# Kernel tuning notes

Measured on AMD Instinct MI355X. Metric: run time of the kernel, lower is better.

## Reference

```python
import jax, jax.numpy as jnp
import numpy as np

D = 512        # input_dim
C = 100        # n_classes
T = 15         # n_trees
DEPTH = 4      # tree_depth
H = 5          # n_heads
ENC = 64       # encoder_dim
GEN = 128      # generator hidden
N_INT = 2 ** DEPTH - 1   # 15 internal nodes
N_LEAF = 2 ** DEPTH      # 16 leaves
TOTAL = T * N_INT * (D + 1) + T * N_LEAF * C + T  # 139440
N_SUP, N_QRY = 4096, 32768


def setup_inputs() -> dict:
    key = jax.random.key(0)
    ks = jax.random.split(key, 8)
    s = lambda k, shp, sc: jax.random.normal(k, shp, jnp.float32) * sc
    return {
        "X_support": s(ks[0], (N_SUP, D), 1.0),
        "X_query": s(ks[1], (N_QRY, D), 1.0),
        # encoder per head: Linear(D,ENC) -> LayerNorm -> GELU -> Linear(ENC,ENC)
        "enc_w1": s(ks[2], (H, D, ENC), 0.5 / np.sqrt(D)),
        "enc_b1": jnp.zeros((H, ENC), jnp.float32),
        "ln_g": jnp.ones((H, ENC), jnp.float32),
        "ln_b": jnp.zeros((H, ENC), jnp.float32),
        "enc_w2": s(ks[3], (H, ENC, ENC), 0.5 / np.sqrt(ENC)),
        "enc_b2": jnp.zeros((H, ENC), jnp.float32),
        # generator per head: Linear(ENC,GEN) -> GELU -> Linear(GEN,TOTAL)
        "gen_w1": s(ks[4], (H, ENC, GEN), 0.5 / np.sqrt(ENC)),
        "gen_b1": jnp.zeros((H, GEN), jnp.float32),
        "gen_w2": s(ks[5], (H, GEN, TOTAL), 0.5 / np.sqrt(GEN)),
        "gen_b2": jnp.zeros((H, TOTAL), jnp.float32),
        "head_weights": jnp.ones((H,), jnp.float32) / H,
        "temperature": jnp.float32(1.0),
    }


def reference(X_support, X_query, enc_w1, enc_b1, ln_g, ln_b, enc_w2, enc_b2,
              gen_w1, gen_b1, gen_w2, gen_b2, head_weights, temperature):
    gelu = lambda x: jax.nn.gelu(x, approximate=False)  # torch nn.GELU default (erf)

    # ---- per-head encoder on support set: [H, S, ENC]
    h1 = jnp.einsum('sd,hde->hse', X_support, enc_w1) + enc_b1[:, None]
    mu = h1.mean(-1, keepdims=True)
    var = h1.var(-1, keepdims=True)  # biased, matches torch LayerNorm
    h1 = (h1 - mu) / jnp.sqrt(var + 1e-5) * ln_g[:, None] + ln_b[:, None]
    enc = jnp.einsum('hse,hef->hsf', gelu(h1), enc_w2) + enc_b2[:, None]
    ctx = enc.mean(axis=1)  # [H, ENC]  (mean over support dim, keepdim squeezed)

    # ---- per-head generator -> tree parameters
    g = gelu(jnp.einsum('he,heg->hg', ctx, gen_w1) + gen_b1)
    params = jnp.tanh(jnp.einsum('hg,hgp->hp', g, gen_w2) + gen_b2) * 2.0  # [H, TOTAL]

    i0 = T * N_INT * D
    i1 = i0 + T * N_INT
    i2 = i1 + T * N_LEAF * C
    split_w = params[:, :i0].reshape(H, T, N_INT, D)
    split_b = params[:, i0:i1].reshape(H, T, N_INT)
    leaf_logits = params[:, i1:i2].reshape(H, T, N_LEAF, C)
    tree_w = jax.nn.softmax(params[:, i2:i2 + T], axis=-1)  # [H, T]

    temp = jnp.clip(temperature, 0.1, 2.0)

    # ---- all node decisions in one pass: [H, Q, T, N_INT]
    dec = jax.nn.sigmoid(
        (jnp.einsum('qd,htnd->hqtn', X_query, split_w) + split_b[:, None]) / temp)

    # ---- bitwise reach propagation level by level (fixed DEPTH=4 loop)
    Q = X_query.shape[0]
    reach = jnp.ones((H, Q, T, 1), X_query.dtype)
    for d in range(DEPTH):
        n = 2 ** d
        start = n - 1
        dlev = dec[..., start:start + n]  # [H,Q,T,n]
        # interleave (left, right) per parent, matching torch new_reach ordering
        reach = jnp.stack([reach * (1.0 - dlev), reach * dlev], axis=-1)
        reach = reach.reshape(H, Q, T, 2 * n)
    # reach: [H, Q, T, N_LEAF]

    leaf_probs = jax.nn.softmax(leaf_logits / temp, axis=-1)  # [H,T,L,C]
    hw = jax.nn.softmax(head_weights)
    # fuse tree mixing and head mixing into one contraction -> [Q, C]
    return jnp.einsum('hqtl,htlc,ht,h->qc', reach, leaf_probs, tree_w, hw)
```

## Files before the change

kernel.cpp:

```cpp
#include <hip/hip_runtime.h>


#define TOTAL 139440
#define I0 115200
#define I1 115425
#define I2 139425
#define NPAIR 38

typedef _Float16 f16;
typedef _Float16 f16x8 __attribute__((ext_vector_type(8)));
typedef _Float16 f16x4 __attribute__((ext_vector_type(4)));
typedef float f32x16 __attribute__((ext_vector_type(16)));

__global__ __launch_bounds__(256) void k1_encode(
    const float* __restrict__ Xs, const float* __restrict__ w1,
    const float* __restrict__ b1, const float* __restrict__ lng,
    const float* __restrict__ lnb, const float* __restrict__ w2,
    float* __restrict__ ctx_sum)
{
  const int h = blockIdx.y;
  const int tid = threadIdx.x;
  const int lane = tid & 63;
  const int wave = tid >> 6;
  const int s0 = blockIdx.x * 64 + wave * 16;
  __shared__ float lsg[4][64];

  float w2r[64];
  #pragma unroll
  for (int e = 0; e < 64; ++e) w2r[e] = w2[(h * 64 + e) * 64 + lane];

  float acc[16];
  #pragma unroll
  for (int r = 0; r < 16; ++r) acc[r] = 0.f;

  const float* wp = w1 + h * 512 * 64;
  for (int d4 = 0; d4 < 128; ++d4) {
    const int d = d4 * 4;
    const float wa = wp[(d + 0) * 64 + lane];
    const float wb = wp[(d + 1) * 64 + lane];
    const float wc = wp[(d + 2) * 64 + lane];
    const float wd = wp[(d + 3) * 64 + lane];
    #pragma unroll
    for (int r = 0; r < 16; ++r) {
      const float4 x4 = *(const float4*)(Xs + (s0 + r) * 512 + d);
      acc[r] = fmaf(x4.x, wa, acc[r]);
      acc[r] = fmaf(x4.y, wb, acc[r]);
      acc[r] = fmaf(x4.z, wc, acc[r]);
      acc[r] = fmaf(x4.w, wd, acc[r]);
    }
  }

  const float bb = b1[h * 64 + lane];
  const float ge = lng[h * 64 + lane];
  const float be = lnb[h * 64 + lane];
  float ctxacc = 0.f;

  for (int r = 0; r < 16; ++r) {
    const float v = acc[r] + bb;
    float s = v, s2 = v * v;
    #pragma unroll
    for (int m = 1; m < 64; m <<= 1) {
      s  += __shfl_xor(s, m, 64);
      s2 += __shfl_xor(s2, m, 64);
    }
    const float mu = s * (1.f / 64.f);
    const float var = fmaxf(s2 * (1.f / 64.f) - mu * mu, 0.f);
    const float y = (v - mu) * rsqrtf(var + 1e-5f) * ge + be;
    const float gl = 0.5f * y * (1.f + erff(y * 0.70710678118654752f));
    lsg[wave][lane] = gl;
    float sm = 0.f;
    #pragma unroll
    for (int e4 = 0; e4 < 16; ++e4) {
      const float4 g4 = *(const float4*)(&lsg[wave][e4 * 4]);
      sm = fmaf(g4.x, w2r[e4 * 4 + 0], sm);
      sm = fmaf(g4.y, w2r[e4 * 4 + 1], sm);
      sm = fmaf(g4.z, w2r[e4 * 4 + 2], sm);
      sm = fmaf(g4.w, w2r[e4 * 4 + 3], sm);
    }
    ctxacc += sm;
  }
  atomicAdd(&ctx_sum[h * 64 + lane], ctxacc);
}

__global__ __launch_bounds__(256) void k2_ctx(
    const float* __restrict__ eb2, const float* __restrict__ gw1,
    const float* __restrict__ gb1, const float* __restrict__ hwin,
    const float* __restrict__ tempin, const float* __restrict__ ctx_sum,
    float* __restrict__ g_out, float* __restrict__ hwit)
{
  __shared__ float ctx[320];
  const int tid = threadIdx.x;
  for (int i = tid; i < 320; i += 256)
    ctx[i] = ctx_sum[i] * (1.f / 4096.f) + eb2[i];
  __syncthreads();
  for (int i = tid; i < 640; i += 256) {
    const int h = i >> 7, j = i & 127;
    float a = gb1[i];
    for (int e = 0; e < 64; ++e)
      a = fmaf(ctx[h * 64 + e], gw1[(h * 64 + e) * 128 + j], a);
    g_out[i] = 0.5f * a * (1.f + erff(a * 0.70710678118654752f));
  }
  if (tid == 0) {
    float m = hwin[0];
    for (int i = 1; i < 5; ++i) m = fmaxf(m, hwin[i]);
    float ex[5]; float se = 0.f;
    for (int i = 0; i < 5; ++i) { ex[i] = __expf(hwin[i] - m); se += ex[i]; }
    for (int i = 0; i < 5; ++i) hwit[i] = ex[i] / se;
    float tp = tempin[0];
    tp = fminf(fmaxf(tp, 0.1f), 2.0f);
    hwit[5] = 1.0f / tp;
  }
}

__global__ __launch_bounds__(256) void k3_params(
    const float* __restrict__ gv, const float* __restrict__ gw2,
    const float* __restrict__ gb2, float* __restrict__ params)
{
  const int h = blockIdx.y;
  __shared__ float gl[128];
  const int tid = threadIdx.x;
  if (tid < 128) gl[tid] = gv[h * 128 + tid];
  __syncthreads();
  const long i4 = (long)blockIdx.x * 256 + tid;
  if (i4 >= TOTAL / 4) return;
  const long i = i4 * 4;
  const float* wp = gw2 + (long)h * 128 * TOTAL + i;
  float4 a = *(const float4*)(gb2 + (long)h * TOTAL + i);
  #pragma unroll 4
  for (int k = 0; k < 128; ++k) {
    const float4 w4 = *(const float4*)(wp + (long)k * TOTAL);
    const float gk = gl[k];
    a.x = fmaf(gk, w4.x, a.x);
    a.y = fmaf(gk, w4.y, a.y);
    a.z = fmaf(gk, w4.z, a.z);
    a.w = fmaf(gk, w4.w, a.w);
  }
  float4 o;
  o.x = 2.f * tanhf(a.x);
  o.y = 2.f * tanhf(a.y);
  o.z = 2.f * tanhf(a.z);
  o.w = 2.f * tanhf(a.w);
  *(float4*)(params + (long)h * TOTAL + i) = o;
}

__global__ __launch_bounds__(256) void k4a_packw(
    const float* __restrict__ params, f16* __restrict__ wpk)
{
  const int t0 = blockIdx.x * 256 + threadIdx.x;
  const int lane = t0 & 63;
  const int kk = (t0 >> 6) & 31;
  const int pair = t0 >> 11;
  const int cl = lane & 31;
  const int tree = pair * 2 + (cl >> 4);
  const int n = cl & 15;
  f16x8 v;
  if (tree < 75 && n < 15) {
    const int h = tree / 15;
    const int t = tree - h * 15;
    const int dbase = kk * 16 + (lane >> 5) * 8;
    const float* src = params + (long)h * TOTAL + ((t * 15 + n) * 512 + dbase);
    const float4 x0 = *(const float4*)(src);
    const float4 x1 = *(const float4*)(src + 4);
    v[0] = (f16)x0.x; v[1] = (f16)x0.y; v[2] = (f16)x0.z; v[3] = (f16)x0.w;
    v[4] = (f16)x1.x; v[5] = (f16)x1.y; v[6] = (f16)x1.z; v[7] = (f16)x1.w;
  } else {
    #pragma unroll
    for (int j = 0; j < 8; ++j) v[j] = (f16)0.f;
  }
  *(f16x8*)(wpk + (long)t0 * 8) = v;
}

__global__ __launch_bounds__(128) void k4b_w2(
    const float* __restrict__ params, const float* __restrict__ hwit,
    f16* __restrict__ w2pk)
{
  const int g = blockIdx.x >> 4;
  const int leaf = blockIdx.x & 15;
  const int h = g / 15, t = g - h * 15;
  const float it = hwit[5];
  float m = -1e30f;
  float tl[15];
  #pragma unroll
  for (int i = 0; i < 15; ++i) {
    tl[i] = params[(long)h * TOTAL + I2 + i];
    m = fmaxf(m, tl[i]);
  }
  float se = 0.f;
  #pragma unroll
  for (int i = 0; i < 15; ++i) se += __expf(tl[i] - m);
  const float tw = __expf(tl[t] - m) / se;
  const float scale = tw * hwit[h];

  const int c = threadIdx.x;
  __shared__ float red[128];
  float lg = -1e30f;
  if (c < 100) lg = params[(long)h * TOTAL + I1 + ((t * 16 + leaf) * 100 + c)] * it;
  red[c] = lg;
  __syncthreads();
  for (int s = 64; s > 0; s >>= 1) {
    if (c < s) red[c] = fmaxf(red[c], red[c + s]);
    __syncthreads();
  }
  const float mx = red[0];
  __syncthreads();
  const float exv = (c < 100) ? __expf(lg - mx) : 0.f;
  red[c] = exv;
  __syncthreads();
  for (int s = 64; s > 0; s >>= 1) {
    if (c < s) red[c] += red[c + s];
    __syncthreads();
  }
  const float inv = 1.f / red[0];
  if (c < 100) {
    const float val = exv * inv * scale;
    const int ln = ((leaf >> 3) << 5) | (c & 31);
    const int j = leaf & 7;
    const int ct = c >> 5;
    w2pk[(((long)g * 4 + ct) * 64 + ln) * 8 + j] = (f16)val;
  }
}

__global__ __launch_bounds__(256, 2) void k5_query(
    const float* __restrict__ Xq, const float* __restrict__ params,
    const f16* __restrict__ wpk, const f16* __restrict__ w2pk,
    const float* __restrict__ hwit, float* __restrict__ out)
{
  __shared__ __align__(16) f16 xf[32 * 64 * 8];
  __shared__ float decs[4][32][34];
  __shared__ float ored[4][1024];

  const int tid = threadIdx.x;
  const int lane = tid & 63;
  const int wave = tid >> 6;
  const int qbase = blockIdx.x * 32;
  const float it = hwit[5];
  const int col = lane & 31;
  const int khalf = lane >> 5;

  {
    const int q = tid >> 3;
    const int db = (tid & 7) * 4;
    const float* xr = Xq + (long)(qbase + q) * 512;
    #pragma unroll
    for (int i = 0; i < 16; ++i) {
      const int d = db + i * 32;
      const float4 x4 = *(const float4*)(xr + d);
      const int kk = d >> 4;
      const int ln = q + 32 * ((d & 15) >> 3);
      const int j0 = d & 7;
      f16x4 v;
      v[0] = (f16)x4.x; v[1] = (f16)x4.y; v[2] = (f16)x4.z; v[3] = (f16)x4.w;
      *(f16x4*)(&xf[(kk * 64 + ln) * 8 + j0]) = v;
    }
  }
  __syncthreads();

  f32x16 oacc[4];
  #pragma unroll
  for (int ct = 0; ct < 4; ++ct)
    #pragma unroll
    for (int r = 0; r < 16; ++r) oacc[ct][r] = 0.f;

  auto process = [&](const f32x16& S0, const f32x16& S1, int pp) {
    const int tree = pp * 2 + (col >> 4);
    const int treec = (tree < 75) ? tree : 74;
    const int hh2 = treec / 15;
    const int tt2 = treec - hh2 * 15;
    const float bn = params[(long)hh2 * TOTAL + I0 + tt2 * 15 + (col & 15)];
    #pragma unroll
    for (int r = 0; r < 16; ++r) {
      const float z = (S0[r] + S1[r] + bn) * it;
      const float dv = 1.f / (1.f + __expf(-z));
      const int row = (r & 3) + 8 * (r >> 2) + 4 * khalf;
      decs[wave][row][col] = dv;
    }
    #pragma unroll
    for (int tf = 0; tf < 2; ++tf) {
      const int g = pp * 2 + tf;
      if (g < 75) {
        const int cb = tf * 16;
        const float* dsr = &decs[wave][col][cb];
        const float d0v = dsr[0];
        const float f0 = khalf ? d0v : 1.f - d0v;
        const float d1v = dsr[1 + khalf];
        const float p10 = f0 * (1.f - d1v);
        const float p11 = f0 * d1v;
        const float d2a = dsr[3 + 2 * khalf];
        const float d2b = dsr[4 + 2 * khalf];
        float p2[4];
        p2[0] = p10 * (1.f - d2a);
        p2[1] = p10 * d2a;
        p2[2] = p11 * (1.f - d2b);
        p2[3] = p11 * d2b;
        float d3[4];
        #pragma unroll
        for (int u = 0; u < 4; ++u) d3[u] = dsr[7 + 4 * khalf + u];
        f16x8 rf;
        #pragma unroll
        for (int mm = 0; mm < 8; ++mm) {
          const float rv = p2[mm >> 1] * ((mm & 1) ? d3[mm >> 1] : (1.f - d3[mm >> 1]));
          rf[mm] = (f16)rv;
        }
        const f16x8* w2p = (const f16x8*)w2pk + ((long)g * 4) * 64 + lane;
        oacc[0] = __builtin_amdgcn_mfma_f32_32x32x16_f16(rf, w2p[0],   oacc[0], 0, 0, 0);
        oacc[1] = __builtin_amdgcn_mfma_f32_32x32x16_f16(rf, w2p[64],  oacc[1], 0, 0, 0);
        oacc[2] = __builtin_amdgcn_mfma_f32_32x32x16_f16(rf, w2p[128], oacc[2], 0, 0, 0);
        oacc[3] = __builtin_amdgcn_mfma_f32_32x32x16_f16(rf, w2p[192], oacc[3], 0, 0, 0);
      }
    }
  };

  for (int p = wave; p < NPAIR; p += 8) {
    const bool has2 = (p + 4 < NPAIR);
    const f16x8* wha = (const f16x8*)wpk + (long)p * 32 * 64 + lane;
    const f16x8* whb = has2 ? ((const f16x8*)wpk + (long)(p + 4) * 32 * 64 + lane) : wha;
    f32x16 Sa0, Sa1, Sb0, Sb1;
    #pragma unroll
    for (int r = 0; r < 16; ++r) { Sa0[r] = 0.f; Sa1[r] = 0.f; Sb0[r] = 0.f; Sb1[r] = 0.f; }
    #pragma unroll
    for (int kk = 0; kk < 32; kk += 2) {
      const f16x8 af0 = *(const f16x8*)(&xf[(kk * 64 + lane) * 8]);
      const f16x8 af1 = *(const f16x8*)(&xf[((kk + 1) * 64 + lane) * 8]);
      const f16x8 wa0 = wha[(long)kk * 64];
      const f16x8 wa1 = wha[(long)(kk + 1) * 64];
      const f16x8 wb0 = whb[(long)kk * 64];
      const f16x8 wb1 = whb[(long)(kk + 1) * 64];
      Sa0 = __builtin_amdgcn_mfma_f32_32x32x16_f16(af0, wa0, Sa0, 0, 0, 0);
      Sb0 = __builtin_amdgcn_mfma_f32_32x32x16_f16(af0, wb0, Sb0, 0, 0, 0);
      Sa1 = __builtin_amdgcn_mfma_f32_32x32x16_f16(af1, wa1, Sa1, 0, 0, 0);
      Sb1 = __builtin_amdgcn_mfma_f32_32x32x16_f16(af1, wb1, Sb1, 0, 0, 0);
    }
    process(Sa0, Sa1, p);
    if (has2) process(Sb0, Sb1, p + 4);
  }

  __syncthreads();
  #pragma unroll
  for (int ct = 0; ct < 4; ++ct) {
    #pragma unroll
    for (int r = 0; r < 16; ++r) {
      const int row = (r & 3) + 8 * (r >> 2) + 4 * khalf;
      ored[wave][row * 32 + col] = oacc[ct][r];
    }
    __syncthreads();
    for (int e = tid; e < 1024; e += 256) {
      const float sm = ored[0][e] + ored[1][e] + ored[2][e] + ored[3][e];
      const int q = e >> 5;
      const int c = ct * 32 + (e & 31);
      if (c < 100) out[(long)(qbase + q) * 100 + c] = sm;
    }
    __syncthreads();
  }
}

extern "C" void kernel_launch(void* const* d_in, const int* in_sizes, int n_in,
                              void* d_out, int out_size, void* d_ws, size_t ws_size,
                              hipStream_t stream) {
  (void)in_sizes; (void)n_in; (void)out_size; (void)ws_size;
  const float* Xs  = (const float*)d_in[0];
  const float* Xq  = (const float*)d_in[1];
  const float* ew1 = (const float*)d_in[2];
  const float* eb1 = (const float*)d_in[3];
  const float* lng = (const float*)d_in[4];
  const float* lnb = (const float*)d_in[5];
  const float* ew2 = (const float*)d_in[6];
  const float* eb2 = (const float*)d_in[7];
  const float* gw1 = (const float*)d_in[8];
  const float* gb1 = (const float*)d_in[9];
  const float* gw2 = (const float*)d_in[10];
  const float* gb2 = (const float*)d_in[11];
  const float* hwi = (const float*)d_in[12];
  const float* tmp = (const float*)d_in[13];
  float* out = (float*)d_out;

  char* ws = (char*)d_ws;
  float* params = (float*)(ws);
  f16*   wpk    = (f16*)(ws + 2788800);
  f16*   w2pk   = (f16*)(ws + 2788800 + 1245184);
  float* ctxs   = (float*)(ws + 4341184);
  float* gbuf   = (float*)(ws + 4342464);
  float* hwit   = (float*)(ws + 4345024);

  hipMemsetAsync(ctxs, 0, 1280, stream);
  hipMemsetAsync(w2pk, 0, 307200, stream);

  k1_encode<<<dim3(64, 5), 256, 0, stream>>>(Xs, ew1, eb1, lng, lnb, ew2, ctxs);
  k2_ctx<<<1, 256, 0, stream>>>(eb2, gw1, gb1, hwi, tmp, ctxs, gbuf, hwit);
  k3_params<<<dim3(137, 5), 256, 0, stream>>>(gbuf, gw2, gb2, params);
  k4a_packw<<<304, 256, 0, stream>>>(params, wpk);
  k4b_w2<<<1200, 128, 0, stream>>>(params, hwit, w2pk);
  k5_query<<<1024, 256, 0, stream>>>(Xq, params, wpk, w2pk, hwit, out);
}
```

Before: 1.040 ms.

## Stream split weights into LDS via async global_load_lds with double-buffered prefetch

The query kernel now stages the packed split-weight tiles into a per-wave LDS ring buffer using direct global-to-LDS loads. It prefetches two k-steps ahead and the next pair's first tiles before running the sigmoid/reach processing, with the split biases preloaded up front. Shared memory is merged into one buffer that aliases the decision and output-reduction regions. Separately, the encoder grid is doubled with half the rows per wave, and the generator loop unroll is raised to 8. The manual waitcnt handling and LDS aliasing add correctness risk, and the larger LDS footprint may reduce occupancy.

```diff
diff --git a/kernel.cpp b/kernel.cpp
--- a/kernel.cpp
+++ b/kernel.cpp
@@ -12,6 +12,12 @@
 typedef _Float16 f16x4 __attribute__((ext_vector_type(4)));
 typedef float f32x16 __attribute__((ext_vector_type(16)));
 
+__device__ __forceinline__ void stage1k(const f16* gsrc, f16* ldst) {
+  __builtin_amdgcn_global_load_lds(
+      (const __attribute__((address_space(1))) unsigned int*)gsrc,
+      (__attribute__((address_space(3))) unsigned int*)ldst, 16, 0, 0);
+}
+
 __global__ __launch_bounds__(256) void k1_encode(
     const float* __restrict__ Xs, const float* __restrict__ w1,
     const float* __restrict__ b1, const float* __restrict__ lng,
@@ -22,16 +28,16 @@
   const int tid = threadIdx.x;
   const int lane = tid & 63;
   const int wave = tid >> 6;
-  const int s0 = blockIdx.x * 64 + wave * 16;
+  const int s0 = blockIdx.x * 32 + wave * 8;
   __shared__ float lsg[4][64];
 
   float w2r[64];
   #pragma unroll
   for (int e = 0; e < 64; ++e) w2r[e] = w2[(h * 64 + e) * 64 + lane];
 
-  float acc[16];
-  #pragma unroll
-  for (int r = 0; r < 16; ++r) acc[r] = 0.f;
+  float acc[8];
+  #pragma unroll
+  for (int r = 0; r < 8; ++r) acc[r] = 0.f;
 
   const float* wp = w1 + h * 512 * 64;
   for (int d4 = 0; d4 < 128; ++d4) {
@@ -41,7 +47,7 @@
     const float wc = wp[(d + 2) * 64 + lane];
     const float wd = wp[(d + 3) * 64 + lane];
     #pragma unroll
-    for (int r = 0; r < 16; ++r) {
+    for (int r = 0; r < 8; ++r) {
       const float4 x4 = *(const float4*)(Xs + (s0 + r) * 512 + d);
       acc[r] = fmaf(x4.x, wa, acc[r]);
       acc[r] = fmaf(x4.y, wb, acc[r]);
@@ -55,7 +61,7 @@
   const float be = lnb[h * 64 + lane];
   float ctxacc = 0.f;
 
-  for (int r = 0; r < 16; ++r) {
+  for (int r = 0; r < 8; ++r) {
     const float v = acc[r] + bb;
     float s = v, s2 = v * v;
     #pragma unroll
@@ -126,7 +132,7 @@
   const long i = i4 * 4;
   const float* wp = gw2 + (long)h * 128 * TOTAL + i;
   float4 a = *(const float4*)(gb2 + (long)h * TOTAL + i);
-  #pragma unroll 4
+  #pragma unroll 8
   for (int k = 0; k < 128; ++k) {
     const float4 w4 = *(const float4*)(wp + (long)k * TOTAL);
     const float gk = gl[k];
@@ -225,9 +231,10 @@
     const f16* __restrict__ wpk, const f16* __restrict__ w2pk,
     const float* __restrict__ hwit, float* __restrict__ out)
 {
-  __shared__ __align__(16) f16 xf[32 * 64 * 8];
-  __shared__ float decs[4][32][34];
-  __shared__ float ored[4][1024];
+  __shared__ __align__(16) unsigned char smem[66048];
+  f16* xf    = (f16*)smem;
+  f16* strm  = (f16*)(smem + 32768);
+  float* du  = (float*)(smem + 49152);
 
   const int tid = threadIdx.x;
   const int lane = tid & 63;
@@ -253,33 +260,43 @@
       *(f16x4*)(&xf[(kk * 64 + ln) * 8 + j0]) = v;
     }
   }
-  __syncthreads();
-
-  f32x16 oacc[4];
-  #pragma unroll
-  for (int ct = 0; ct < 4; ++ct)
-    #pragma unroll
-    for (int r = 0; r < 16; ++r) oacc[ct][r] = 0.f;
-
-  auto process = [&](const f32x16& S0, const f32x16& S1, int pp) {
+
+  auto load_bias = [&](int pp) -> float {
     const int tree = pp * 2 + (col >> 4);
     const int treec = (tree < 75) ? tree : 74;
     const int hh2 = treec / 15;
     const int tt2 = treec - hh2 * 15;
-    const float bn = params[(long)hh2 * TOTAL + I0 + tt2 * 15 + (col & 15)];
+    return params[(long)hh2 * TOTAL + I0 + tt2 * 15 + (col & 15)];
+  };
+  float bnA[5], bnB[5];
+  #pragma unroll
+  for (int i = 0; i < 5; ++i) {
+    const int p = wave + 8 * i;
+    bnA[i] = load_bias(p);
+    bnB[i] = (p + 4 < NPAIR) ? load_bias(p + 4) : 0.f;
+  }
+  __syncthreads();
+
+  f32x16 oacc[4];
+  #pragma unroll
+  for (int ct = 0; ct < 4; ++ct)
+    #pragma unroll
+    for (int r = 0; r < 16; ++r) oacc[ct][r] = 0.f;
+
+  auto process = [&](const f32x16& S0, const f32x16& S1, int pp, float bn) {
     #pragma unroll
     for (int r = 0; r < 16; ++r) {
       const float z = (S0[r] + S1[r] + bn) * it;
       const float dv = 1.f / (1.f + __expf(-z));
       const int row = (r & 3) + 8 * (r >> 2) + 4 * khalf;
-      decs[wave][row][col] = dv;
+      du[wave * 1056 + row * 33 + col] = dv;
     }
     #pragma unroll
     for (int tf = 0; tf < 2; ++tf) {
       const int g = pp * 2 + tf;
       if (g < 75) {
         const int cb = tf * 16;
-        const float* dsr = &decs[wave][col][cb];
+        const float* dsr = &du[wave * 1056 + col * 33 + cb];
         const float d0v = dsr[0];
         const float f0 = khalf ? d0v : 1.f - d0v;
         const float d1v = dsr[1 + khalf];
@@ -310,28 +327,61 @@
     }
   };
 
-  for (int p = wave; p < NPAIR; p += 8) {
+  f16* sb = strm + wave * 2048;
+
+  const f16* wpa = wpk + (long)wave * 16384;
+  const f16* wpb = wpk + (long)(wave + 4) * 16384;
+  stage1k(wpa + 0 * 512 + lane * 8, sb + 0 * 512);
+  stage1k(wpb + 0 * 512 + lane * 8, sb + 1 * 512);
+  stage1k(wpa + 1 * 512 + lane * 8, sb + 2 * 512);
+  stage1k(wpb + 1 * 512 + lane * 8, sb + 3 * 512);
+
+  #pragma unroll 1
+  for (int i = 0; i < 5; ++i) {
+    const int p = wave + 8 * i;
     const bool has2 = (p + 4 < NPAIR);
-    const f16x8* wha = (const f16x8*)wpk + (long)p * 32 * 64 + lane;
-    const f16x8* whb = has2 ? ((const f16x8*)wpk + (long)(p + 4) * 32 * 64 + lane) : wha;
     f32x16 Sa0, Sa1, Sb0, Sb1;
     #pragma unroll
     for (int r = 0; r < 16; ++r) { Sa0[r] = 0.f; Sa1[r] = 0.f; Sb0[r] = 0.f; Sb1[r] = 0.f; }
-    #pragma unroll
-    for (int kk = 0; kk < 32; kk += 2) {
-      const f16x8 af0 = *(const f16x8*)(&xf[(kk * 64 + lane) * 8]);
-      const f16x8 af1 = *(const f16x8*)(&xf[((kk + 1) * 64 + lane) * 8]);
-      const f16x8 wa0 = wha[(long)kk * 64];
-      const f16x8 wa1 = wha[(long)(kk + 1) * 64];
-      const f16x8 wb0 = whb[(long)kk * 64];
-      const f16x8 wb1 = whb[(long)(kk + 1) * 64];
-      Sa0 = __builtin_amdgcn_mfma_f32_32x32x16_f16(af0, wa0, Sa0, 0, 0, 0);
-      Sb0 = __builtin_amdgcn_mfma_f32_32x32x16_f16(af0, wb0, Sb0, 0, 0, 0);
-      Sa1 = __builtin_amdgcn_mfma_f32_32x32x16_f16(af1, wa1, Sa1, 0, 0, 0);
-      Sb1 = __builtin_amdgcn_mfma_f32_32x32x16_f16(af1, wb1, Sb1, 0, 0, 0);
-    }
-    process(Sa0, Sa1, p);
-    if (has2) process(Sb0, Sb1, p + 4);
+
+    #pragma unroll
+    for (int kk = 0; kk < 32; ++kk) {
+      if (kk < 31) asm volatile("s_waitcnt vmcnt(2)" ::: "memory");
+      else         asm volatile("s_waitcnt vmcnt(0)" ::: "memory");
+      const int s0 = (2 * kk) & 3;
+      const f16x8 af = *(const f16x8*)(&xf[(kk * 64 + lane) * 8]);
+      const f16x8 Ba = *(const f16x8*)(&sb[(s0 + 0) * 512 + lane * 8]);
+      const f16x8 Bb = *(const f16x8*)(&sb[(s0 + 1) * 512 + lane * 8]);
+      if (kk & 1) {
+        Sa1 = __builtin_amdgcn_mfma_f32_32x32x16_f16(af, Ba, Sa1, 0, 0, 0);
+        Sb1 = __builtin_amdgcn_mfma_f32_32x32x16_f16(af, Bb, Sb1, 0, 0, 0);
+      } else {
+        Sa0 = __builtin_amdgcn_mfma_f32_32x32x16_f16(af, Ba, Sa0, 0, 0, 0);
+        Sb0 = __builtin_amdgcn_mfma_f32_32x32x16_f16(af, Bb, Sb0, 0, 0, 0);
+      }
+      asm volatile("s_waitcnt lgkmcnt(0)" ::: "memory");
+      if (kk < 30) {
+        stage1k(wpa + (kk + 2) * 512 + lane * 8, sb + (s0 + 0) * 512);
+        stage1k(wpb + (kk + 2) * 512 + lane * 8, sb + (s0 + 1) * 512);
+      }
+    }
+
+    const f16* wpa2 = wpa;
+    const f16* wpb2 = wpb;
+    if (i < 4) {
+      const int pn = p + 8;
+      wpa2 = wpk + (long)pn * 16384;
+      wpb2 = wpk + (long)(pn + 4) * 16384;
+      stage1k(wpa2 + 0 * 512 + lane * 8, sb + 0 * 512);
+      stage1k(wpb2 + 0 * 512 + lane * 8, sb + 1 * 512);
+      stage1k(wpa2 + 1 * 512 + lane * 8, sb + 2 * 512);
+      stage1k(wpb2 + 1 * 512 + lane * 8, sb + 3 * 512);
+    }
+
+    process(Sa0, Sa1, p, bnA[i]);
+    if (has2) process(Sb0, Sb1, p + 4, bnB[i]);
+
+    wpa = wpa2; wpb = wpb2;
   }
 
   __syncthreads();
@@ -340,11 +390,11 @@
     #pragma unroll
     for (int r = 0; r < 16; ++r) {
       const int row = (r & 3) + 8 * (r >> 2) + 4 * khalf;
-      ored[wave][row * 32 + col] = oacc[ct][r];
+      du[wave * 1024 + row * 32 + col] = oacc[ct][r];
     }
     __syncthreads();
     for (int e = tid; e < 1024; e += 256) {
-      const float sm = ored[0][e] + ored[1][e] + ored[2][e] + ored[3][e];
+      const float sm = du[e] + du[1024 + e] + du[2048 + e] + du[3072 + e];
       const int q = e >> 5;
       const int c = ct * 32 + (e & 31);
       if (c < 100) out[(long)(qbase + q) * 100 + c] = sm;
@@ -384,7 +434,7 @@
   hipMemsetAsync(ctxs, 0, 1280, stream);
   hipMemsetAsync(w2pk, 0, 307200, stream);
 
-  k1_encode<<<dim3(64, 5), 256, 0, stream>>>(Xs, ew1, eb1, lng, lnb, ew2, ctxs);
+  k1_encode<<<dim3(128, 5), 256, 0, stream>>>(Xs, ew1, eb1, lng, lnb, ew2, ctxs);
   k2_ctx<<<1, 256, 0, stream>>>(eb2, gw1, gb1, hwi, tmp, ctxs, gbuf, hwit);
   k3_params<<<dim3(137, 5), 256, 0, stream>>>(gbuf, gw2, gb2, params);
   k4a_packw<<<304, 256, 0, stream>>>(params, wpk);
```

Measured after the change: 998.7 us. 1.04x faster.
